# Kernel tuning notes

Measured on AMD Instinct MI355X. Metric: run time of the kernel, lower is better.

## Reference

```python
import jax, jax.numpy as jnp
import numpy as np

R = 16
SEQ_LEN = 96
D_MODEL = 512
D_FF = 2048


def tr_linear(x2d, in_cores, out_cores, bias):
    # Tensor-ring linear: W[i1..im, o1..on] = Tr(G1[i1]...Gm[im] H1[o1]...Hn[on])
    # y = x @ W.reshape(prod(in), prod(out)) + bias, computed without forming W fully.
    b = x2d.shape[0]
    in_dims = tuple(c.shape[1] for c in in_cores)
    t = x2d.reshape((b,) + in_dims)
    # fold input modes into the ring: s ends as [b, r0, r_m]
    s = jnp.tensordot(t, in_cores[0], axes=[[1], [1]])  # [b, i2..im, r0, r1]
    for core in in_cores[1:]:
        s = jnp.einsum('bi...ac,cid->b...ad', s, core)
    # fold output cores into W: [r_m, o1..on, r0]
    W = out_cores[0]
    for core in out_cores[1:]:
        W = jnp.einsum('c...d,dpe->c...pe', W, core)
    # close the ring: trace over (r0, r_m)
    y = jnp.einsum('bac,c...a->b...', s, W)
    return y.reshape(b, -1) + bias


def ffn_forward(x, c1_in2, c1_in3, c1_ind, c1_out_seq, c1_out_ff, b1,
                c2_in_seq, c2_in_ff, c2_out2, c2_out3, c2_outd, b2):
    B, L, D = x.shape
    in1 = list(c1_in2) + [c1_in3, c1_ind]          # factorint(96)+[d_model] modes
    out1 = [c1_out_seq, c1_out_ff]                 # [seq_len, d_ff]
    h = tr_linear(x.reshape(B, L * D), in1, out1, b1)   # [B, seq_len*d_ff]
    h = jax.nn.relu(h)                             # dropout = identity (eval mode)
    in2 = [c2_in_seq, c2_in_ff]
    out2 = list(c2_out2) + [c2_out3, c2_outd]
    y = tr_linear(h, in2, out2, b2)                # [B, seq_len*d_model]
    return y.reshape(B, L, D)                      # output.view(x.shape)


def setup_inputs():
    key = jax.random.key(0)
    ks = jax.random.split(key, 13)
    s = 0.2  # core init scale keeps 9-core ring products near unit magnitude
    return {
        'x': jax.random.normal(ks[0], (64, SEQ_LEN, D_MODEL), jnp.float32),
        'c1_in2': s * jax.random.normal(ks[1], (5, R, 2, R), jnp.float32),
        'c1_in3': s * jax.random.normal(ks[2], (R, 3, R), jnp.float32),
        'c1_ind': s * jax.random.normal(ks[3], (R, D_MODEL, R), jnp.float32),
        'c1_out_seq': s * jax.random.normal(ks[4], (R, SEQ_LEN, R), jnp.float32),
        'c1_out_ff': s * jax.random.normal(ks[5], (R, D_FF, R), jnp.float32),
        'b1': 0.01 * jax.random.normal(ks[6], (SEQ_LEN * D_FF,), jnp.float32),
        'c2_in_seq': s * jax.random.normal(ks[7], (R, SEQ_LEN, R), jnp.float32),
        'c2_in_ff': s * jax.random.normal(ks[8], (R, D_FF, R), jnp.float32),
        'c2_out2': s * jax.random.normal(ks[9], (5, R, 2, R), jnp.float32),
        'c2_out3': s * jax.random.normal(ks[10], (R, 3, R), jnp.float32),
        'c2_outd': s * jax.random.normal(ks[11], (R, D_MODEL, R), jnp.float32),
        'b2': 0.01 * jax.random.normal(ks[12], (SEQ_LEN * D_MODEL,), jnp.float32),
    }


def reference(x, c1_in2, c1_in3, c1_ind, c1_out_seq, c1_out_ff, b1,
              c2_in_seq, c2_in_ff, c2_out2, c2_out3, c2_outd, b2):
    return ffn_forward(x, c1_in2, c1_in3, c1_ind, c1_out_seq, c1_out_ff, b1,
                       c2_in_seq, c2_in_ff, c2_out2, c2_out3, c2_outd, b2)
```

## Files before the change

### kernel.cpp

```cpp
#include <hip/hip_runtime.h>


typedef _Float16 f16;
typedef f16 f16x8 __attribute__((ext_vector_type(8)));
typedef f16 f16x4 __attribute__((ext_vector_type(4)));
typedef float f32x4 __attribute__((ext_vector_type(4)));

__device__ __forceinline__ void gload16(const void* g, void* l) {
    __builtin_amdgcn_global_load_lds(
        (const __attribute__((address_space(1))) void*)g,
        (__attribute__((address_space(3))) void*)l, 16, 0, 0);
}

__global__ void build_chain2_kernel(const float* __restrict__ a5, const float* __restrict__ a3,
                                    const float* __restrict__ b5, const float* __restrict__ b3,
                                    float* __restrict__ Pout, float* __restrict__ Qout) {
    __shared__ float Ma[256], Mb[256];
    const int l = blockIdx.x % 96, chain = blockIdx.x / 96;
    const float* G5 = chain ? b5 : a5;
    const float* G3 = chain ? b3 : a3;
    float* out = chain ? Qout : Pout;
    const int i6 = l % 3, lh = l / 3;
    const int dig[5] = {(lh >> 4) & 1, (lh >> 3) & 1, (lh >> 2) & 1, (lh >> 1) & 1, lh & 1};
    const int a = threadIdx.x >> 4, bn = threadIdx.x & 15;
    Ma[threadIdx.x] = G5[a * 32 + dig[0] * 16 + bn];
    __syncthreads();
    float* cur = Ma; float* nxt = Mb;
    for (int g = 1; g < 5; ++g) {
        float s = 0.f;
        #pragma unroll
        for (int r = 0; r < 16; ++r)
            s += cur[a * 16 + r] * G5[g * 512 + r * 32 + dig[g] * 16 + bn];
        nxt[threadIdx.x] = s;
        __syncthreads();
        float* t = cur; cur = nxt; nxt = t;
    }
    float s = 0.f;
    #pragma unroll
    for (int r = 0; r < 16; ++r)
        s += cur[a * 16 + r] * G3[r * 48 + i6 * 16 + bn];
    out[(a * 96 + l) * 16 + bn] = s;
}

__device__ __forceinline__ void permM_body(const float* __restrict__ in, f16* __restrict__ bh,
                                           int K, int q, int k0, float* t) {
    const float* src = in + ((size_t)q * K + k0) * 16;
    for (int i = threadIdx.x; i < 1024; i += 256)
        ((float4*)t)[i] = ((const float4*)src)[i];
    __syncthreads();
    const int j = threadIdx.x >> 4, kc = (threadIdx.x & 15) * 16;
    f16* dh = bh + (size_t)(q * 16 + j) * K + k0 + kc;
    f16 vh[16];
    #pragma unroll
    for (int i = 0; i < 16; ++i) vh[i] = (f16)t[(kc + i) * 16 + j];
    *(f16x8*)(dh) = *(f16x8*)&vh[0]; *(f16x8*)(dh + 8) = *(f16x8*)&vh[8];
}
__device__ __forceinline__ void permO_body(const float* __restrict__ in, f16* __restrict__ bh,
                                           int N, int blk) {
    const int idx = blk * 256 + threadIdx.x;
    const int n = idx >> 8, k = idx & 255;
    bh[idx] = (f16)in[((k >> 4) * N + n) * 16 + (k & 15)];
}
__global__ void prep_bt_kernel(const float* __restrict__ c1_ind, const float* __restrict__ c1_off,
                               const float* __restrict__ c2_iff, const float* __restrict__ c2_outd,
                               f16* BT1h, f16* BT2h, f16* BT3h, f16* BT4h) {
    __shared__ float t[4096];
    int b = blockIdx.x;
    if (b < 32)   { permM_body(c1_ind, BT1h, 512,  b & 15, (b >> 4) * 256, t); return; }
    b -= 32;
    if (b < 128)  { permM_body(c2_iff, BT3h, 2048, b & 15, (b >> 4) * 256, t); return; }
    b -= 128;
    if (b < 2048) { permO_body(c1_off, BT2h, 2048, b); return; }
    b -= 2048;
    permO_body(c2_outd, BT4h, 512, b);
}

__global__ void xsplit_kernel(const float* __restrict__ x, f16* __restrict__ xh) {
    const int idx = blockIdx.x * 256 + threadIdx.x;
    const float4 v = ((const float4*)x)[idx];
    f16x4 hh;
    hh[0] = (f16)v.x; hh[1] = (f16)v.y; hh[2] = (f16)v.z; hh[3] = (f16)v.w;
    ((f16x4*)xh)[idx] = hh;
}

__global__ void sfold_kernel(const f16* __restrict__ z, const float* __restrict__ P,
                             float* __restrict__ spart2) {
    __shared__ f16 zs[4096];
    __shared__ float Ps[4096];
    const int b = blockIdx.x, lc = blockIdx.y, sk = blockIdx.z, tid = threadIdx.x;
    const int r0 = tid >> 4, rE = tid & 15;
    for (int i = tid; i < 4096; i += 256) {
        const int rp = i & 15, r = (i >> 4) & 15, l = i >> 8;
        Ps[i] = P[((size_t)rp * 96 + lc * 16 + l) * 16 + r];
    }
    const f16x8* zsrc = (const f16x8*)(z + ((size_t)sk * 6144 + b * 96 + lc * 16) * 256);
    for (int i = tid; i < 512; i += 256) ((f16x8*)zs)[i] = zsrc[i];
    __syncthreads();
    float acc = 0.f;
    #pragma unroll
    for (int l = 0; l < 16; ++l)
        #pragma unroll
        for (int r = 0; r < 16; ++r)
            acc += (float)zs[l * 256 + r * 16 + rE] * Ps[(l * 16 + r) * 16 + r0];
    spart2[(((size_t)sk * 6 + lc) * 64 + b) * 256 + tid] = acc;
}

__global__ void sred_kernel(const float* __restrict__ spart2, float* __restrict__ sfin,
                            int nsl) {
    const int b = blockIdx.x, tid = threadIdx.x;
    float acc = 0.f;
    #pragma unroll 8
    for (int s = 0; s < nsl; ++s) acc += spart2[((size_t)s * 64 + b) * 256 + tid];
    sfin[b * 256 + tid] = acc;
}

__global__ void uexpand_kernel(const float* __restrict__ sfin, const float* __restrict__ O,
                               f16* __restrict__ uh) {
    __shared__ float s_sh[256], o_sh[256];
    const int o1 = blockIdx.x, b = blockIdx.y, tid = threadIdx.x;
    s_sh[tid] = sfin[b * 256 + tid];
    o_sh[tid] = O[((tid >> 4) * 96 + o1) * 16 + (tid & 15)];
    __syncthreads();
    const int dd = tid >> 4, a = tid & 15;
    float acc = 0.f;
    #pragma unroll
    for (int c = 0; c < 16; ++c) acc += s_sh[a * 16 + c] * o_sh[c * 16 + dd];
    uh[((size_t)b * 96 + o1) * 256 + tid] = (f16)acc;
}

template<int EPI>
__global__ __launch_bounds__(256, 4) void trgemm_kernel(
    const f16* __restrict__ Ah, const f16* __restrict__ BTh,
    const float* __restrict__ bias,
    float* __restrict__ Cf, f16* __restrict__ Ch,
    int M, int N, int K, int kchunk)
{
    __shared__ f16 As[8192];
    __shared__ f16 Bs[8192];
    const int n0 = blockIdx.x * 128, m0 = blockIdx.y * 128;
    const int kbase = blockIdx.z * kchunk;
    const int tid = threadIdx.x;
    const int w = tid >> 6, lane = tid & 63;
    const int wm = w >> 1, wn = w & 1;
    const int lr = lane & 15, lq = lane >> 4;

    const int ra = 2 * w;
    size_t aoff0 = (size_t)(m0 + ra * 16 + lr) * K + kbase + lq * 8;
    size_t aoff1 = aoff0 + (size_t)16 * K;
    size_t boff0 = (size_t)(n0 + ra * 16 + lr) * K + kbase + lq * 8;
    size_t boff1 = boff0 + (size_t)16 * K;

    f32x4 acc[4][4];
    #pragma unroll
    for (int i = 0; i < 4; ++i)
        #pragma unroll
        for (int j = 0; j < 4; ++j) acc[i][j] = (f32x4)0.f;

    const int nkt = kchunk >> 6;
    for (int kt = 0; kt < nkt; ++kt) {
        __syncthreads();
        #pragma unroll
        for (int c = 0; c < 2; ++c) {
            gload16(Ah + aoff0 + c * 32, &As[(ra + 0) * 1024 + c * 512]);
            gload16(Ah + aoff1 + c * 32, &As[(ra + 1) * 1024 + c * 512]);
            gload16(BTh + boff0 + c * 32, &Bs[(ra + 0) * 1024 + c * 512]);
            gload16(BTh + boff1 + c * 32, &Bs[(ra + 1) * 1024 + c * 512]);
        }
        aoff0 += 64; aoff1 += 64; boff0 += 64; boff1 += 64;
        __syncthreads();
        #pragma unroll
        for (int ks = 0; ks < 2; ++ks) {
            f16x8 afh[4], bfh[4];
            #pragma unroll
            for (int mf = 0; mf < 4; ++mf)
                afh[mf] = *(const f16x8*)&As[(wm * 4 + mf) * 1024 + ks * 512 + lane * 8];
            #pragma unroll
            for (int nf = 0; nf < 4; ++nf)
                bfh[nf] = *(const f16x8*)&Bs[(wn * 4 + nf) * 1024 + ks * 512 + lane * 8];
            #pragma unroll
            for (int mf = 0; mf < 4; ++mf)
                #pragma unroll
                for (int nf = 0; nf < 4; ++nf)
                    acc[mf][nf] = __builtin_amdgcn_mfma_f32_16x16x32_f16(afh[mf], bfh[nf], acc[mf][nf], 0, 0, 0);
        }
    }

    #pragma unroll
    for (int mf = 0; mf < 4; ++mf)
        #pragma unroll
        for (int nf = 0; nf < 4; ++nf)
            #pragma unroll
            for (int r = 0; r < 4; ++r) {
                const int row = m0 + wm * 64 + mf * 16 + lq * 4 + r;
                const int col = n0 + wn * 64 + nf * 16 + lr;
                float v = acc[mf][nf][r];
                if constexpr (EPI == 0) {
                    Ch[((size_t)blockIdx.z * M + row) * N + col] = (f16)v;
                } else {
                    v += bias[(size_t)(row % 96) * N + col];
                    if constexpr (EPI == 1) {
                        v = fmaxf(v, 0.f);
                        Ch[(size_t)row * N + col] = (f16)v;
                    } else {
                        Cf[(size_t)row * N + col] = v;
                    }
                }
            }
}

extern "C" void kernel_launch(void* const* d_in, const int* in_sizes, int n_in,
                              void* d_out, int out_size, void* d_ws, size_t ws_size,
                              hipStream_t stream) {
    const float* x        = (const float*)d_in[0];
    const float* c1_in2   = (const float*)d_in[1];
    const float* c1_in3   = (const float*)d_in[2];
    const float* c1_ind   = (const float*)d_in[3];
    const float* c1_oseq  = (const float*)d_in[4];
    const float* c1_off   = (const float*)d_in[5];
    const float* b1       = (const float*)d_in[6];
    const float* c2_iseq  = (const float*)d_in[7];
    const float* c2_iff   = (const float*)d_in[8];
    const float* c2_out2  = (const float*)d_in[9];
    const float* c2_out3  = (const float*)d_in[10];
    const float* c2_outd  = (const float*)d_in[11];
    const float* b2       = (const float*)d_in[12];
    float* out = (float*)d_out;

    char* base = (char*)d_ws;
    float* Pseq1 = (float*)base;
    float* Qseq2 = (float*)(base + 98304);
    f16*   BT1h  = (f16*)(base + 196608);
    f16*   BT2h  = BT1h + 2 * 131072;
    f16*   BT3h  = BT2h + 2 * 524288;
    f16*   BT4h  = BT3h + 2 * 524288;
    char*  hreg  = base + 5439488;
    f16*   hh    = (f16*)hreg;
    f16*   xh    = (f16*)hreg;
    float* spart2= (float*)(hreg + 25165824);
    float* sfin  = (float*)(hreg + 28311552);
    char*  zreg  = base + 55771136;
    f16*   zp    = (f16*)zreg;
    f16*   uh    = (f16*)zreg;

    const int SK = 8;

    build_chain2_kernel<<<192, 256, 0, stream>>>(c1_in2, c1_in3, c2_out2, c2_out3, Pseq1, Qseq2);
    prep_bt_kernel<<<2720, 256, 0, stream>>>(c1_ind, c1_off, c2_iff, c2_outd,
                                             BT1h, BT2h, BT3h, BT4h);
    xsplit_kernel<<<3072, 256, 0, stream>>>(x, xh);

    trgemm_kernel<0><<<dim3(2, 48, SK), 256, 0, stream>>>(xh, BT1h, nullptr,
                                                          nullptr, zp, 6144, 256, 512, 512 / SK);
    sfold_kernel<<<dim3(64, 6, SK), 256, 0, stream>>>(zp, Pseq1, spart2);
    sred_kernel<<<64, 256, 0, stream>>>(spart2, sfin, 6 * SK);
    uexpand_kernel<<<dim3(96, 64), 256, 0, stream>>>(sfin, c1_oseq, uh);
    trgemm_kernel<1><<<dim3(16, 48, 1), 256, 0, stream>>>(uh, BT2h, b1,
                                                          nullptr, hh, 6144, 2048, 256, 256);
    trgemm_kernel<0><<<dim3(2, 48, SK), 256, 0, stream>>>(hh, BT3h, nullptr,
                                                          nullptr, zp, 6144, 256, 2048, 2048 / SK);
    sfold_kernel<<<dim3(64, 6, SK), 256, 0, stream>>>(zp, c2_iseq, spart2);
    sred_kernel<<<64, 256, 0, stream>>>(spart2, sfin, 6 * SK);
    uexpand_kernel<<<dim3(96, 64), 256, 0, stream>>>(sfin, Qseq2, uh);
    trgemm_kernel<2><<<dim3(4, 48, 1), 256, 0, stream>>>(uh, BT4h, b2,
                                                         out, nullptr, 6144, 512, 256, 256);
}
```

Before: 245.0 us.

## Fuse partial-sum reduction with u-expansion and pre-permute fold matrices

Merges the split-K reduction kernel and the u-expansion kernel into one kernel. Each block reduces the partial sums for one batch row once and then expands 24 output positions from a shared-memory copy of the output core. The P matrices used by the fold step are now stored in a pre-transposed layout, written by the chain-build kernel, so the fold kernel can load them with contiguous float4 copies instead of strided gathers. This removes two launches and the intermediate buffer. In exchange, the expand stage runs only 256 blocks, and each one redundantly re-reduces 48 partial slices.

```diff
diff --git a/kernel.cpp b/kernel.cpp
--- a/kernel.cpp
+++ b/kernel.cpp
@@ -14,15 +14,22 @@
 
 __global__ void build_chain2_kernel(const float* __restrict__ a5, const float* __restrict__ a3,
                                     const float* __restrict__ b5, const float* __restrict__ b3,
-                                    float* __restrict__ Pout, float* __restrict__ Qout) {
+                                    const float* __restrict__ c2_iseq,
+                                    float* __restrict__ Pout, float* __restrict__ Qout,
+                                    float* __restrict__ P2c) {
     __shared__ float Ma[256], Mb[256];
-    const int l = blockIdx.x % 96, chain = blockIdx.x / 96;
+    const int blk = blockIdx.x;
+    const int a = threadIdx.x >> 4, bn = threadIdx.x & 15;
+    if (blk >= 192) {
+        const int l = blk - 192;
+        P2c[l * 256 + bn * 16 + a] = c2_iseq[(a * 96 + l) * 16 + bn];
+        return;
+    }
+    const int l = blk % 96, chain = blk / 96;
     const float* G5 = chain ? b5 : a5;
     const float* G3 = chain ? b3 : a3;
-    float* out = chain ? Qout : Pout;
     const int i6 = l % 3, lh = l / 3;
     const int dig[5] = {(lh >> 4) & 1, (lh >> 3) & 1, (lh >> 2) & 1, (lh >> 1) & 1, lh & 1};
-    const int a = threadIdx.x >> 4, bn = threadIdx.x & 15;
     Ma[threadIdx.x] = G5[a * 32 + dig[0] * 16 + bn];
     __syncthreads();
     float* cur = Ma; float* nxt = Mb;
@@ -39,7 +46,8 @@
     #pragma unroll
     for (int r = 0; r < 16; ++r)
         s += cur[a * 16 + r] * G3[r * 48 + i6 * 16 + bn];
-    out[(a * 96 + l) * 16 + bn] = s;
+    if (chain == 0) Pout[l * 256 + bn * 16 + a] = s;
+    else            Qout[(a * 96 + l) * 16 + bn] = s;
 }
 
 __device__ __forceinline__ void permM_body(const float* __restrict__ in, f16* __restrict__ bh,
@@ -83,16 +91,14 @@
     ((f16x4*)xh)[idx] = hh;
 }
 
-__global__ void sfold_kernel(const f16* __restrict__ z, const float* __restrict__ P,
+__global__ void sfold_kernel(const f16* __restrict__ z, const float* __restrict__ P2,
                              float* __restrict__ spart2) {
     __shared__ f16 zs[4096];
     __shared__ float Ps[4096];
     const int b = blockIdx.x, lc = blockIdx.y, sk = blockIdx.z, tid = threadIdx.x;
     const int r0 = tid >> 4, rE = tid & 15;
-    for (int i = tid; i < 4096; i += 256) {
-        const int rp = i & 15, r = (i >> 4) & 15, l = i >> 8;
-        Ps[i] = P[((size_t)rp * 96 + lc * 16 + l) * 16 + r];
-    }
+    const float4* psrc = (const float4*)(P2 + lc * 4096);
+    for (int i = tid; i < 1024; i += 256) ((float4*)Ps)[i] = psrc[i];
     const f16x8* zsrc = (const f16x8*)(z + ((size_t)sk * 6144 + b * 96 + lc * 16) * 256);
     for (int i = tid; i < 512; i += 256) ((f16x8*)zs)[i] = zsrc[i];
     __syncthreads();
@@ -105,27 +111,28 @@
     spart2[(((size_t)sk * 6 + lc) * 64 + b) * 256 + tid] = acc;
 }
 
-__global__ void sred_kernel(const float* __restrict__ spart2, float* __restrict__ sfin,
-                            int nsl) {
-    const int b = blockIdx.x, tid = threadIdx.x;
+__global__ void sexpand_kernel(const float* __restrict__ spart2, const float* __restrict__ O,
+                               f16* __restrict__ uh) {
+    __shared__ float s_sh[272];
+    __shared__ float o_sh[6144];
+    const int b = blockIdx.x, og = blockIdx.y, tid = threadIdx.x;
     float acc = 0.f;
     #pragma unroll 8
-    for (int s = 0; s < nsl; ++s) acc += spart2[((size_t)s * 64 + b) * 256 + tid];
-    sfin[b * 256 + tid] = acc;
-}
-
-__global__ void uexpand_kernel(const float* __restrict__ sfin, const float* __restrict__ O,
-                               f16* __restrict__ uh) {
-    __shared__ float s_sh[256], o_sh[256];
-    const int o1 = blockIdx.x, b = blockIdx.y, tid = threadIdx.x;
-    s_sh[tid] = sfin[b * 256 + tid];
-    o_sh[tid] = O[((tid >> 4) * 96 + o1) * 16 + (tid & 15)];
+    for (int s = 0; s < 48; ++s) acc += spart2[((size_t)s * 64 + b) * 256 + tid];
+    s_sh[(tid >> 4) * 17 + (tid & 15)] = acc;
+    for (int i = tid; i < 6144; i += 256) {
+        const int c = i / 384, rem = i - c * 384;
+        o_sh[i] = O[c * 1536 + og * 384 + rem];
+    }
     __syncthreads();
     const int dd = tid >> 4, a = tid & 15;
-    float acc = 0.f;
-    #pragma unroll
-    for (int c = 0; c < 16; ++c) acc += s_sh[a * 16 + c] * o_sh[c * 16 + dd];
-    uh[((size_t)b * 96 + o1) * 256 + tid] = (f16)acc;
+    #pragma unroll
+    for (int o1 = 0; o1 < 24; ++o1) {
+        float u = 0.f;
+        #pragma unroll
+        for (int c = 0; c < 16; ++c) u += s_sh[a * 17 + c] * o_sh[c * 384 + o1 * 16 + dd];
+        uh[((size_t)b * 96 + og * 24 + o1) * 256 + tid] = (f16)u;
+    }
 }
 
 template<int EPI>
@@ -237,14 +244,15 @@
     f16*   hh    = (f16*)hreg;
     f16*   xh    = (f16*)hreg;
     float* spart2= (float*)(hreg + 25165824);
-    float* sfin  = (float*)(hreg + 28311552);
+    float* P2c   = (float*)(hreg + 28311552);
     char*  zreg  = base + 55771136;
     f16*   zp    = (f16*)zreg;
     f16*   uh    = (f16*)zreg;
 
     const int SK = 8;
 
-    build_chain2_kernel<<<192, 256, 0, stream>>>(c1_in2, c1_in3, c2_out2, c2_out3, Pseq1, Qseq2);
+    build_chain2_kernel<<<288, 256, 0, stream>>>(c1_in2, c1_in3, c2_out2, c2_out3,
+                                                 c2_iseq, Pseq1, Qseq2, P2c);
     prep_bt_kernel<<<2720, 256, 0, stream>>>(c1_ind, c1_off, c2_iff, c2_outd,
                                              BT1h, BT2h, BT3h, BT4h);
     xsplit_kernel<<<3072, 256, 0, stream>>>(x, xh);
@@ -252,15 +260,13 @@
     trgemm_kernel<0><<<dim3(2, 48, SK), 256, 0, stream>>>(xh, BT1h, nullptr,
                                                           nullptr, zp, 6144, 256, 512, 512 / SK);
     sfold_kernel<<<dim3(64, 6, SK), 256, 0, stream>>>(zp, Pseq1, spart2);
-    sred_kernel<<<64, 256, 0, stream>>>(spart2, sfin, 6 * SK);
-    uexpand_kernel<<<dim3(96, 64), 256, 0, stream>>>(sfin, c1_oseq, uh);
+    sexpand_kernel<<<dim3(64, 4), 256, 0, stream>>>(spart2, c1_oseq, uh);
     trgemm_kernel<1><<<dim3(16, 48, 1), 256, 0, stream>>>(uh, BT2h, b1,
                                                           nullptr, hh, 6144, 2048, 256, 256);
     trgemm_kernel<0><<<dim3(2, 48, SK), 256, 0, stream>>>(hh, BT3h, nullptr,
                                                           nullptr, zp, 6144, 256, 2048, 2048 / SK);
-    sfold_kernel<<<dim3(64, 6, SK), 256, 0, stream>>>(zp, c2_iseq, spart2);
-    sred_kernel<<<64, 256, 0, stream>>>(spart2, sfin, 6 * SK);
-    uexpand_kernel<<<dim3(96, 64), 256, 0, stream>>>(sfin, Qseq2, uh);
+    sfold_kernel<<<dim3(64, 6, SK), 256, 0, stream>>>(zp, P2c, spart2);
+    sexpand_kernel<<<dim3(64, 4), 256, 0, stream>>>(spart2, Qseq2, uh);
     trgemm_kernel<2><<<dim3(4, 48, 1), 256, 0, stream>>>(uh, BT4h, b2,
                                                          out, nullptr, 6144, 512, 256, 256);
 }
```

After: 230.0 us. -6.1%, faster.
